# Kernel optimization log

Hardware: AMD Instinct MI355X
Metric: run time of the kernel (lower is better)

Reference implementation:

```python
import jax, jax.numpy as jnp
import numpy as np

N = 262144          # total atoms
B = 2048            # graphs (batch.max()+1)
HID = 256           # hidden
CND = 128           # cond_proj_dim
K = 16              # n_clusters
PH = 8              # pool_heads
DH = HID // PH      # head_dim


def setup_inputs() -> dict:
    key = jax.random.key(0)
    ks = jax.random.split(key, 20)
    s = 0.02
    inp = {
        "h_atom": jax.random.normal(ks[0], (N, HID), jnp.float32),
        "c_atom": jax.random.normal(ks[1], (N, CND), jnp.float32),
        "batch": jnp.sort(jax.random.randint(ks[2], (N,), 0, B)).astype(jnp.int64),
        # gate: Linear(HID+CND, HID) -> GELU -> Linear(HID, 1) -> Sigmoid
        "W1": jax.random.normal(ks[3], (HID + CND, HID), jnp.float32) * s,
        "b1": jnp.zeros((HID,), jnp.float32),
        "W2": jax.random.normal(ks[4], (HID, 1), jnp.float32) * s,
        "b2": jnp.zeros((1,), jnp.float32),
        # assign: Linear(HID, HID) -> GELU -> Linear(HID, K)
        "A1": jax.random.normal(ks[5], (HID, HID), jnp.float32) * s,
        "ab1": jnp.zeros((HID,), jnp.float32),
        "A2": jax.random.normal(ks[6], (HID, K), jnp.float32) * s,
        "ab2": jnp.zeros((K,), jnp.float32),
        # cluster_proj: Linear(HID, HID)
        "Wc": jax.random.normal(ks[7], (HID, HID), jnp.float32) * s,
        "bc": jnp.zeros((HID,), jnp.float32),
        # readout
        "q": jax.random.normal(ks[8], (PH, DH), jnp.float32),   # readout_q param
        "Wk": jax.random.normal(ks[9], (HID, HID), jnp.float32) * s,
        "Wv": jax.random.normal(ks[10], (HID, HID), jnp.float32) * s,
        # LayerNorm
        "gamma": jnp.ones((HID,), jnp.float32),
        "beta": jnp.zeros((HID,), jnp.float32),
    }
    return inp


def reference(h_atom, c_atom, batch, W1, b1, W2, b2, A1, ab1, A2, ab2,
              Wc, bc, q, Wk, Wv, gamma, beta):
    gelu = lambda x: jax.nn.gelu(x, approximate=False)  # torch default GELU (erf)
    # Stage 1: condition-aware gating
    g = gelu(jnp.concatenate([h_atom, c_atom], axis=-1) @ W1 + b1)
    alpha = jax.nn.sigmoid(g @ W2 + b2)                 # [N, 1]
    h_gated = alpha * h_atom                            # [N, HID]
    # Stage 2: soft cluster assignment
    S = jax.nn.softmax(gelu(h_gated @ A1 + ab1) @ A2 + ab2, axis=-1)  # [N, K]
    # Ragged per-graph segment matmul: cluster[b,k,:] = sum_{n in graph b} S[n,k] * h_gated[n,:]
    cluster = jnp.stack(
        [jax.ops.segment_sum(h_gated * S[:, k:k + 1], batch, num_segments=B)
         for k in range(K)], axis=1)                    # [B, K, HID]
    cluster = cluster @ Wc + bc                         # cluster_proj
    # Stage 3: multi-head attention readout over K clusters
    Kp = (cluster @ Wk).reshape(B, K, PH, DH)
    Vp = (cluster @ Wv).reshape(B, K, PH, DH)
    scale = DH ** -0.5
    logits = jnp.einsum('pd,bkpd->bpk', q, Kp) * scale  # [B, PH, K]
    w = jax.nn.softmax(logits, axis=-1)                 # dropout p=0 -> identity
    out = jnp.einsum('bpk,bkpd->bpd', w, Vp).reshape(B, HID)
    # LayerNorm (eps = 1e-5, torch default)
    mu = out.mean(axis=-1, keepdims=True)
    var = ((out - mu) ** 2).mean(axis=-1, keepdims=True)
    return (out - mu) * jax.lax.rsqrt(var + 1e-5) * gamma + beta
```

## Files before the change

### kernel.cpp

```cpp
#include <hip/hip_runtime.h>
#include <hip/hip_bf16.h>
#include <math.h>
#include <stdint.h>

#define NATOMS 262144
#define BGRAPH 2048
#define CHUNK 10240

typedef __bf16 bf16_t;
typedef __bf16 bf16x8 __attribute__((ext_vector_type(8)));
typedef __bf16 bf16x4 __attribute__((ext_vector_type(4)));
typedef float f32x4 __attribute__((ext_vector_type(4)));

__device__ __forceinline__ float bf2f(bf16_t x){ return (float)x; }

__device__ __forceinline__ float gelu_f(float x){
    float s  = x * 0.70710678118654752f;
    float a  = fabsf(s);
    float t  = __builtin_amdgcn_rcpf(fmaf(0.3275911f, a, 1.0f));
    float p  = t * fmaf(t, fmaf(t, fmaf(t, fmaf(t, 1.061405429f, -1.453152027f),
                                        1.421413741f), -0.284496736f), 0.254829592f);
    float e  = __expf(-a * a);
    float er = copysignf(fmaf(-p, e, 1.0f), s);
    return 0.5f * x * (1.0f + er);
}

__device__ __forceinline__ void gl_lds16(const void* g, void* l){
    __attribute__((address_space(3))) uint32_t* lp =
        reinterpret_cast<__attribute__((address_space(3))) uint32_t*>(
            reinterpret_cast<uintptr_t>(l));
    __builtin_amdgcn_global_load_lds(static_cast<const uint32_t*>(g), lp, 16, 0, 0);
}

#define PREP_W1 10
#define PREP_A1 394
#define PREP_WC 650
#define PREP_WK 906
#define PREP_WV 1162
#define PREP_A2 1418
#define PREP_C  1434
#define PREP_END 3482

__device__ __forceinline__ void chunk_tr(const void* src, bf16_t* dst, int Kd, int idx, int bf){
    if (idx >= Kd * 256) return;
    int k = idx >> 8, n = idx & 255;
    bf16_t v = bf ? ((const bf16_t*)src)[idx] : (bf16_t)(((const float*)src)[idx]);
    dst[((size_t)(k >> 5) * 256 + n) * 40 + (k & 31)] = v;
}

__global__ void prep_kernel(
    const int* __restrict__ batch, const void* __restrict__ gamma,
    const void* b1, const void* W2, const void* ab1, const void* bc,
    const void* q, const void* beta, const void* ab2, const void* b2,
    const void* W1, const void* A1, const void* Wc, const void* Wk, const void* Wv,
    const void* A2, const void* cnd,
    bf16_t* __restrict__ W1c, bf16_t* __restrict__ A1c, bf16_t* __restrict__ Wcc,
    bf16_t* __restrict__ Wkc, bf16_t* __restrict__ Wvc, bf16_t* __restrict__ A2t,
    float* __restrict__ P, int* __restrict__ flags, int* __restrict__ starts,
    bf16_t* __restrict__ cbOut)
{
    const int tid = threadIdx.x, blk = blockIdx.x;
    const int bf = (((const unsigned*)gamma)[0] == 0x3F803F80u) ? 1 : 0;
    if (blk == 0 && tid == 0) flags[0] = bf;

    if (blk < 9) {
        int b = blk * 256 + tid;
        if (b > BGRAPH) return;
        int is64 = (batch[NATOMS - 1] == 0) ? 1 : 0;
        int lo = 0, hi = NATOMS;
        while (lo < hi) {
            int mid = (lo + hi) >> 1;
            int v = is64 ? batch[2 * mid] : batch[mid];
            if (v < b) lo = mid + 1; else hi = mid;
        }
        starts[b] = lo;
        return;
    }
    if (blk == 9) {
#define CV(p,i) (bf ? bf2f(((const bf16_t*)(p))[i]) : ((const float*)(p))[i])
        P[tid]        = CV(b1, tid);
        P[256 + tid]  = CV(W2, tid);
        P[512 + tid]  = CV(ab1, tid);
        P[768 + tid]  = CV(bc, tid);
        P[1024 + tid] = CV(q, tid);
        P[1280 + tid] = CV(gamma, tid);
        P[1536 + tid] = CV(beta, tid);
        if (tid < 16) P[1792 + tid] = CV(ab2, tid);
        if (tid == 16) P[1808] = CV(b2, 0);
#undef CV
        return;
    }
    if (blk < PREP_A1) { chunk_tr(W1, W1c, 384, (blk - PREP_W1) * 256 + tid, bf); return; }
    if (blk < PREP_WC) { chunk_tr(A1, A1c, 256, (blk - PREP_A1) * 256 + tid, bf); return; }
    if (blk < PREP_WK) { chunk_tr(Wc, Wcc, 256, (blk - PREP_WC) * 256 + tid, bf); return; }
    if (blk < PREP_WV) { chunk_tr(Wk, Wkc, 256, (blk - PREP_WK) * 256 + tid, bf); return; }
    if (blk < PREP_A2) { chunk_tr(Wv, Wvc, 256, (blk - PREP_WV) * 256 + tid, bf); return; }
    if (blk < PREP_C)  {
        int i = (blk - PREP_A2) * 256 + tid;
        if (i >= 256 * 16) return;
        int k = i >> 4, n = i & 15;
        bf16_t v = bf ? ((const bf16_t*)A2)[i] : (bf16_t)(((const float*)A2)[i]);
        A2t[n * 256 + k] = v;
        return;
    }
    if (bf) return;
    size_t i = (size_t)(blk - PREP_C) * 256 + tid;
    const size_t total = (size_t)NATOMS * 128 / 8;
#pragma unroll
    for (int it = 0; it < 8; ++it, i += 524288) {
        if (i >= total) break;
        const float4* s = (const float4*)cnd + i * 2;
        float4 a = s[0], b = s[1];
        bf16x8 v = { (bf16_t)a.x,(bf16_t)a.y,(bf16_t)a.z,(bf16_t)a.w,
                     (bf16_t)b.x,(bf16_t)b.y,(bf16_t)b.z,(bf16_t)b.w };
        *(bf16x8*)(cbOut + i * 8) = v;
    }
}

__global__ __launch_bounds__(512, 2) void atom_kernel(
    const void* __restrict__ h, const void* __restrict__ cnd, const bf16_t* __restrict__ cb,
    const bf16_t* __restrict__ W1c, const bf16_t* __restrict__ A1c,
    const bf16_t* __restrict__ A2t, const float* __restrict__ P,
    const int* __restrict__ flags,
    bf16_t* __restrict__ hg_out, float* __restrict__ S_out)
{
    __shared__ bf16_t ldsX[128 * 264];
    __shared__ bf16_t ldsW[2][2 * CHUNK];
    __shared__ float  ldsV[256];
    __shared__ float  ldsB1[256];
    __shared__ float  ldsAB1[256];
    __shared__ float  ldsAlpha[128];

    const int tid  = threadIdx.x;
    const int wave = tid >> 6;
    const int lane = tid & 63;
    const int quad = lane >> 4;
    const int l15  = lane & 15;
    const int wr   = wave >> 2;
    const int wc   = wave & 3;
    const int a0   = blockIdx.x * 128;
    const int dbf  = flags[0];

    const bf16_t* cbp = dbf ? (const bf16_t*)cnd : cb;

    bf16x8 cf[4][4];
#pragma unroll
    for (int kc = 0; kc < 4; ++kc)
#pragma unroll
        for (int mt = 0; mt < 4; ++mt)
            cf[kc][mt] = *(const bf16x8*)(cbp + (size_t)(a0 + wr * 64 + mt * 16 + l15) * 128 + kc * 32 + quad * 8);

    if (tid < 256) { ldsV[tid] = P[256 + tid]; ldsB1[tid] = P[tid]; ldsAB1[tid] = P[512 + tid]; }
    if (tid < 128) ldsAlpha[tid] = 0.f;
    const float b2v = P[1808];

    if (dbf) {
        const uint4* hs = (const uint4*)((const bf16_t*)h + (size_t)a0 * 256);
#pragma unroll
        for (int i = 0; i < 8; ++i) {
            int lin = i * 512 + tid; int row = lin >> 5; int off = lin & 31;
            *(uint4*)(&ldsX[row * 264 + off * 8]) = hs[row * 32 + off];
        }
    } else {
        const float4* hs = (const float4*)((const float*)h + (size_t)a0 * 256);
#pragma unroll
        for (int i = 0; i < 16; ++i) {
            int lin = i * 512 + tid; int row = lin >> 6; int off = lin & 63;
            float4 v = hs[row * 64 + off];
            bf16x4 w = { (bf16_t)v.x, (bf16_t)v.y, (bf16_t)v.z, (bf16_t)v.w };
            *(bf16x4*)(&ldsX[row * 264 + off * 4]) = w;
        }
    }

    auto stage = [&](int bsel, const bf16_t* src){
#pragma unroll
        for (int i = 0; i < 5; ++i) {
            int u = i * 512 + wave * 64;
            gl_lds16(src + (size_t)(u + lane) * 8, &ldsW[bsel][0] + (size_t)u * 8);
        }
    };

    stage(0, W1c);
    __syncthreads();

    f32x4 acc[4][4];
#pragma unroll
    for (int a = 0; a < 4; ++a)
#pragma unroll
        for (int b = 0; b < 4; ++b) acc[a][b] = (f32x4){0.f,0.f,0.f,0.f};

#pragma unroll
    for (int ks = 0; ks < 6; ++ks) {
        const int cur = ks & 1;
        const bf16_t* nxt = (ks < 5) ? (W1c + (size_t)(ks + 1) * 2 * CHUNK) : A1c;
        stage(cur ^ 1, nxt);
        bf16x8 af[2][4], bv[2][4];
#pragma unroll
        for (int kh = 0; kh < 2; ++kh)
#pragma unroll
            for (int j = 0; j < 4; ++j)
                bv[kh][j] = *(const bf16x8*)(&ldsW[cur][kh * CHUNK + (wc * 64 + j * 16 + l15) * 40 + quad * 8]);
        if (ks < 4) {
#pragma unroll
            for (int kh = 0; kh < 2; ++kh)
#pragma unroll
                for (int mt = 0; mt < 4; ++mt)
                    af[kh][mt] = *(const bf16x8*)(&ldsX[(wr * 64 + mt * 16 + l15) * 264 + ks * 64 + kh * 32 + quad * 8]);
        } else {
#pragma unroll
            for (int kh = 0; kh < 2; ++kh)
#pragma unroll
                for (int mt = 0; mt < 4; ++mt)
                    af[kh][mt] = cf[(ks - 4) * 2 + kh][mt];
        }
        __builtin_amdgcn_s_setprio(1);
#pragma unroll
        for (int kh = 0; kh < 2; ++kh)
#pragma unroll
            for (int mt = 0; mt < 4; ++mt)
#pragma unroll
                for (int j = 0; j < 4; ++j)
                    acc[mt][j] = __builtin_amdgcn_mfma_f32_16x16x32_bf16(af[kh][mt], bv[kh][j], acc[mt][j], 0, 0, 0);
        __builtin_amdgcn_s_setprio(0);
        __syncthreads();
    }

    for (int mt = 0; mt < 4; ++mt) {
        float p[4] = {0.f, 0.f, 0.f, 0.f};
        for (int j = 0; j < 4; ++j) {
            int col = wc * 64 + j * 16 + l15;
            float w = ldsV[col];
            float bb = ldsB1[col];
            for (int r = 0; r < 4; ++r) {
                float g = gelu_f(acc[mt][j][r] + bb);
                p[r] += g * w;
            }
        }
        for (int off = 1; off < 16; off <<= 1)
            for (int r = 0; r < 4; ++r) p[r] += __shfl_xor(p[r], off, 64);
        if (l15 == 0)
            for (int r = 0; r < 4; ++r)
                atomicAdd(&ldsAlpha[wr * 64 + mt * 16 + quad * 4 + r], p[r]);
    }
    __syncthreads();

    {
        int r = tid >> 2, p4 = tid & 3;
        float al = __builtin_amdgcn_rcpf(1.f + __expf(-(ldsAlpha[r] + b2v)));
        bf16_t* xrow = &ldsX[r * 264 + p4 * 64];
        bf16_t* grow = hg_out + (size_t)(a0 + r) * 256 + p4 * 64;
        for (int i = 0; i < 8; ++i) {
            bf16x8 v = *(bf16x8*)(xrow + i * 8);
            for (int e = 0; e < 8; ++e) v[e] = (bf16_t)(bf2f(v[e]) * al);
            *(bf16x8*)(xrow + i * 8) = v;
            *(bf16x8*)(grow + i * 8) = v;
        }
    }
    __syncthreads();

#pragma unroll
    for (int a = 0; a < 4; ++a)
#pragma unroll
        for (int b = 0; b < 4; ++b) acc[a][b] = (f32x4){0.f,0.f,0.f,0.f};
#pragma unroll
    for (int ks = 0; ks < 4; ++ks) {
        const int cur = ks & 1;
        if (ks < 3) stage(cur ^ 1, A1c + (size_t)(ks + 1) * 2 * CHUNK);
        bf16x8 af[2][4], bv[2][4];
#pragma unroll
        for (int kh = 0; kh < 2; ++kh) {
#pragma unroll
            for (int j = 0; j < 4; ++j)
                bv[kh][j] = *(const bf16x8*)(&ldsW[cur][kh * CHUNK + (wc * 64 + j * 16 + l15) * 40 + quad * 8]);
#pragma unroll
            for (int mt = 0; mt < 4; ++mt)
                af[kh][mt] = *(const bf16x8*)(&ldsX[(wr * 64 + mt * 16 + l15) * 264 + ks * 64 + kh * 32 + quad * 8]);
        }
        __builtin_amdgcn_s_setprio(1);
#pragma unroll
        for (int kh = 0; kh < 2; ++kh)
#pragma unroll
            for (int mt = 0; mt < 4; ++mt)
#pragma unroll
                for (int j = 0; j < 4; ++j)
                    acc[mt][j] = __builtin_amdgcn_mfma_f32_16x16x32_bf16(af[kh][mt], bv[kh][j], acc[mt][j], 0, 0, 0);
        __builtin_amdgcn_s_setprio(0);
        __syncthreads();
    }

    for (int mt = 0; mt < 4; ++mt)
        for (int j = 0; j < 4; ++j) {
            int col = wc * 64 + j * 16 + l15;
            float bb = ldsAB1[col];
            for (int r = 0; r < 4; ++r) {
                int row = wr * 64 + mt * 16 + quad * 4 + r;
                ldsX[row * 264 + col] = (bf16_t)gelu_f(acc[mt][j][r] + bb);
            }
        }
    if (tid < 128) {
        int n = tid >> 3, k0 = (tid & 7) * 32;
#pragma unroll
        for (int p = 0; p < 4; ++p)
            *(uint4*)(&ldsW[0][n * 264 + k0 + p * 8]) = *(const uint4*)(A2t + n * 256 + k0 + p * 8);
    }
    __syncthreads();

    f32x4 acc3 = (f32x4){0.f,0.f,0.f,0.f};
#pragma unroll
    for (int ks = 0; ks < 8; ++ks) {
        int kb = ks * 32 + quad * 8;
        bf16x8 a = *(const bf16x8*)(&ldsX[(wave * 16 + l15) * 264 + kb]);
        bf16x8 b = *(const bf16x8*)(&ldsW[0][l15 * 264 + kb]);
        acc3 = __builtin_amdgcn_mfma_f32_16x16x32_bf16(a, b, acc3, 0, 0, 0);
    }
    float ab2v = P[1792 + l15];
    float lv[4], mx[4], ex[4], sm[4];
    for (int r = 0; r < 4; ++r) { lv[r] = acc3[r] + ab2v; mx[r] = lv[r]; }
    for (int off = 1; off < 16; off <<= 1)
        for (int r = 0; r < 4; ++r) { float o = __shfl_xor(mx[r], off, 64); mx[r] = fmaxf(mx[r], o); }
    for (int r = 0; r < 4; ++r) { ex[r] = __expf(lv[r] - mx[r]); sm[r] = ex[r]; }
    for (int off = 1; off < 16; off <<= 1)
        for (int r = 0; r < 4; ++r) sm[r] += __shfl_xor(sm[r], off, 64);
    for (int r = 0; r < 4; ++r) {
        int row = wave * 16 + quad * 4 + r;
        S_out[(size_t)(a0 + row) * 16 + l15] = ex[r] / sm[r];
    }
}

__global__ __launch_bounds__(256) void segment_kernel(
    const bf16_t* __restrict__ hg, const float* __restrict__ S,
    const int* __restrict__ starts, bf16_t* __restrict__ craw)
{
    __shared__ float ldsS[16 * 16];
    int b = blockIdx.x, tid = threadIdx.x;
    int s = starts[b], e = starts[b + 1];
    float acc[16];
#pragma unroll
    for (int k = 0; k < 16; ++k) acc[k] = 0.f;
    for (int n0 = s; n0 < e; n0 += 16) {
        int cnt = min(16, e - n0);
        if (tid < cnt * 16) ldsS[tid] = S[(size_t)(n0 + (tid >> 4)) * 16 + (tid & 15)];
        __syncthreads();
        for (int a = 0; a < cnt; ++a) {
            float v = bf2f(hg[(size_t)(n0 + a) * 256 + tid]);
            const f32x4* sr = (const f32x4*)(&ldsS[a * 16]);
            f32x4 s0 = sr[0], s1 = sr[1], s2 = sr[2], s3 = sr[3];
            acc[0]  += s0[0] * v; acc[1]  += s0[1] * v; acc[2]  += s0[2] * v; acc[3]  += s0[3] * v;
            acc[4]  += s1[0] * v; acc[5]  += s1[1] * v; acc[6]  += s1[2] * v; acc[7]  += s1[3] * v;
            acc[8]  += s2[0] * v; acc[9]  += s2[1] * v; acc[10] += s2[2] * v; acc[11] += s2[3] * v;
            acc[12] += s3[0] * v; acc[13] += s3[1] * v; acc[14] += s3[2] * v; acc[15] += s3[3] * v;
        }
        __syncthreads();
    }
#pragma unroll
    for (int k = 0; k < 16; ++k)
        craw[((size_t)b * 16 + k) * 256 + tid] = (bf16_t)acc[k];
}

__global__ __launch_bounds__(256, 2) void cluster_kernel(
    const bf16_t* __restrict__ A, const bf16_t* __restrict__ Wcc,
    const bf16_t* __restrict__ Wkc, const bf16_t* __restrict__ Wvc,
    const float* __restrict__ P,
    bf16_t* __restrict__ CK, bf16_t* __restrict__ CV)
{
    __shared__ bf16_t ldsA[64 * 264];
    __shared__ bf16_t ldsW[2][CHUNK];
    const int tid = threadIdx.x;
    const int wave = tid >> 6, lane = tid & 63, quad = lane >> 4, l15 = lane & 15;
    const size_t r0 = (size_t)blockIdx.x * 64;
    const float* bias = P + 768;

    auto stage = [&](int bsel, const bf16_t* src){
#pragma unroll
        for (int i = 0; i < 5; ++i) {
            int u = i * 256 + wave * 64;
            gl_lds16(src + (size_t)(u + lane) * 8, &ldsW[bsel][0] + (size_t)u * 8);
        }
    };

    const uint4* as = (const uint4*)(A + r0 * 256);
#pragma unroll
    for (int i = 0; i < 8; ++i) {
        int lin = i * 256 + tid; int row = lin >> 5; int off = lin & 31;
        *(uint4*)(&ldsA[row * 264 + off * 8]) = as[row * 32 + off];
    }
    stage(0, Wcc);
    __syncthreads();

    f32x4 acc[4][4];

#pragma unroll
    for (int a = 0; a < 4; ++a)
#pragma unroll
        for (int b = 0; b < 4; ++b) acc[a][b] = (f32x4){0.f,0.f,0.f,0.f};
#pragma unroll
    for (int ks = 0; ks < 8; ++ks) {
        const int cur = ks & 1;
        const bf16_t* nxt = (ks < 7) ? (Wcc + (size_t)(ks + 1) * CHUNK) : Wkc;
        stage(cur ^ 1, nxt);
        bf16x8 af[4], bv[4];
        int kb = ks * 32 + quad * 8;
#pragma unroll
        for (int j = 0; j < 4; ++j)
            bv[j] = *(const bf16x8*)(&ldsW[cur][(wave * 64 + j * 16 + l15) * 40 + quad * 8]);
#pragma unroll
        for (int mt = 0; mt < 4; ++mt) af[mt] = *(const bf16x8*)(&ldsA[(mt * 16 + l15) * 264 + kb]);
        __builtin_amdgcn_s_setprio(1);
#pragma unroll
        for (int mt = 0; mt < 4; ++mt)
#pragma unroll
            for (int j = 0; j < 4; ++j)
                acc[mt][j] = __builtin_amdgcn_mfma_f32_16x16x32_bf16(af[mt], bv[j], acc[mt][j], 0, 0, 0);
        __builtin_amdgcn_s_setprio(0);
        __syncthreads();
    }
    for (int mt = 0; mt < 4; ++mt)
        for (int j = 0; j < 4; ++j) {
            int col = wave * 64 + j * 16 + l15;
            float bvl = bias[col];
            for (int r = 0; r < 4; ++r)
                ldsA[(mt * 16 + quad * 4 + r) * 264 + col] = (bf16_t)(acc[mt][j][r] + bvl);
        }
    __syncthreads();

#pragma unroll
    for (int a = 0; a < 4; ++a)
#pragma unroll
        for (int b = 0; b < 4; ++b) acc[a][b] = (f32x4){0.f,0.f,0.f,0.f};
#pragma unroll
    for (int ks = 0; ks < 8; ++ks) {
        const int cur = ks & 1;
        const bf16_t* nxt = (ks < 7) ? (Wkc + (size_t)(ks + 1) * CHUNK) : Wvc;
        stage(cur ^ 1, nxt);
        bf16x8 af[4], bv[4];
        int kb = ks * 32 + quad * 8;
#pragma unroll
        for (int j = 0; j < 4; ++j)
            bv[j] = *(const bf16x8*)(&ldsW[cur][(wave * 64 + j * 16 + l15) * 40 + quad * 8]);
#pragma unroll
        for (int mt = 0; mt < 4; ++mt) af[mt] = *(const bf16x8*)(&ldsA[(mt * 16 + l15) * 264 + kb]);
        __builtin_amdgcn_s_setprio(1);
#pragma unroll
        for (int mt = 0; mt < 4; ++mt)
#pragma unroll
            for (int j = 0; j < 4; ++j)
                acc[mt][j] = __builtin_amdgcn_mfma_f32_16x16x32_bf16(af[mt], bv[j], acc[mt][j], 0, 0, 0);
        __builtin_amdgcn_s_setprio(0);
        __syncthreads();
    }
    for (int mt = 0; mt < 4; ++mt)
        for (int j = 0; j < 4; ++j) {
            int col = wave * 64 + j * 16 + l15;
            for (int r = 0; r < 4; ++r)
                CK[(r0 + mt * 16 + quad * 4 + r) * 256 + col] = (bf16_t)acc[mt][j][r];
        }

#pragma unroll
    for (int a = 0; a < 4; ++a)
#pragma unroll
        for (int b = 0; b < 4; ++b) acc[a][b] = (f32x4){0.f,0.f,0.f,0.f};
#pragma unroll
    for (int ks = 0; ks < 8; ++ks) {
        const int cur = ks & 1;
        if (ks < 7) stage(cur ^ 1, Wvc + (size_t)(ks + 1) * CHUNK);
        bf16x8 af[4], bv[4];
        int kb = ks * 32 + quad * 8;
#pragma unroll
        for (int j = 0; j < 4; ++j)
            bv[j] = *(const bf16x8*)(&ldsW[cur][(wave * 64 + j * 16 + l15) * 40 + quad * 8]);
#pragma unroll
        for (int mt = 0; mt < 4; ++mt) af[mt] = *(const bf16x8*)(&ldsA[(mt * 16 + l15) * 264 + kb]);
        __builtin_amdgcn_s_setprio(1);
#pragma unroll
        for (int mt = 0; mt < 4; ++mt)
#pragma unroll
            for (int j = 0; j < 4; ++j)
                acc[mt][j] = __builtin_amdgcn_mfma_f32_16x16x32_bf16(af[mt], bv[j], acc[mt][j], 0, 0, 0);
        __builtin_amdgcn_s_setprio(0);
        __syncthreads();
    }
    for (int mt = 0; mt < 4; ++mt)
        for (int j = 0; j < 4; ++j) {
            int col = wave * 64 + j * 16 + l15;
            for (int r = 0; r < 4; ++r)
                CV[(r0 + mt * 16 + quad * 4 + r) * 256 + col] = (bf16_t)acc[mt][j][r];
        }
}

__global__ __launch_bounds__(256) void attn_ln_kernel(
    const bf16_t* __restrict__ Kp, const bf16_t* __restrict__ Vp,
    const float* __restrict__ P, const int* __restrict__ flags,
    void* __restrict__ out)
{
    __shared__ float lw[8][16];
    __shared__ float w1s[4], w2s[4];
    int b = blockIdx.x, tid = threadIdx.x;
    const int dbf = flags[0];
    const float* q     = P + 1024;
    const float* gamma = P + 1280;
    const float* beta  = P + 1536;
    if (tid < 128) {
        int p = tid >> 4, k = tid & 15;
        const bf16x8* kr = (const bf16x8*)(Kp + ((size_t)b * 16 + k) * 256 + p * 32);
        const float* qr = q + p * 32;
        float dot = 0.f;
#pragma unroll
        for (int i = 0; i < 4; ++i) {
            bf16x8 v = kr[i];
#pragma unroll
            for (int e = 0; e < 8; ++e) dot += qr[i * 8 + e] * bf2f(v[e]);
        }
        lw[p][k] = dot * 0.17677669529663687f;
    }
    __syncthreads();
    if (tid < 8) {
        float m = -1e30f;
        for (int k = 0; k < 16; ++k) m = fmaxf(m, lw[tid][k]);
        float s = 0.f;
        for (int k = 0; k < 16; ++k) { float ev = __expf(lw[tid][k] - m); lw[tid][k] = ev; s += ev; }
        float inv = 1.f / s;
        for (int k = 0; k < 16; ++k) lw[tid][k] *= inv;
    }
    __syncthreads();
    int p = tid >> 5, d = tid & 31;
    float o = 0.f;
    for (int k = 0; k < 16; ++k)
        o += lw[p][k] * bf2f(Vp[((size_t)b * 16 + k) * 256 + p * 32 + d]);
    float s1 = o, s2 = o * o;
    for (int off = 1; off < 64; off <<= 1) { s1 += __shfl_xor(s1, off, 64); s2 += __shfl_xor(s2, off, 64); }
    int wv = tid >> 6;
    if ((tid & 63) == 0) { w1s[wv] = s1; w2s[wv] = s2; }
    __syncthreads();
    float ts1 = w1s[0] + w1s[1] + w1s[2] + w1s[3];
    float ts2 = w2s[0] + w2s[1] + w2s[2] + w2s[3];
    float mu = ts1 * (1.f / 256.f);
    float var = ts2 * (1.f / 256.f) - mu * mu;
    float y = (o - mu) * rsqrtf(var + 1e-5f) * gamma[tid] + beta[tid];
    if (dbf) ((bf16_t*)out)[(size_t)b * 256 + tid] = (bf16_t)y;
    else     ((float*)out)[(size_t)b * 256 + tid]  = y;
}

extern "C" void kernel_launch(void* const* d_in, const int* in_sizes, int n_in,
                              void* d_out, int out_size, void* d_ws, size_t ws_size,
                              hipStream_t stream) {
    const void* h     = d_in[0];
    const void* cnd   = d_in[1];
    const int*  batch = (const int*)d_in[2];
    const void* W1    = d_in[3];
    const void* b1    = d_in[4];
    const void* W2    = d_in[5];
    const void* b2    = d_in[6];
    const void* A1    = d_in[7];
    const void* ab1   = d_in[8];
    const void* A2    = d_in[9];
    const void* ab2   = d_in[10];
    const void* Wc    = d_in[11];
    const void* bc    = d_in[12];
    const void* q     = d_in[13];
    const void* Wk    = d_in[14];
    const void* Wv    = d_in[15];
    const void* gamma = d_in[16];
    const void* beta  = d_in[17];

    char* ws = (char*)d_ws;
    size_t off = 0;
    bf16_t* W1c  = (bf16_t*)(ws + off); off += 12 * CHUNK * 2;
    bf16_t* A1c  = (bf16_t*)(ws + off); off += 8 * CHUNK * 2;
    bf16_t* Wcc  = (bf16_t*)(ws + off); off += 8 * CHUNK * 2;
    bf16_t* Wkc  = (bf16_t*)(ws + off); off += 8 * CHUNK * 2;
    bf16_t* Wvc  = (bf16_t*)(ws + off); off += 8 * CHUNK * 2;
    bf16_t* A2t  = (bf16_t*)(ws + off); off += 8192;
    float*  P    = (float*)(ws + off);  off += 8192;
    int*    flags = (int*)(ws + off);   off += 256;
    int*    starts = (int*)(ws + off);  off += 8448;
    float*  S    = (float*)(ws + off);  off += (size_t)NATOMS * 16 * 4;
    bf16_t* hg   = (bf16_t*)(ws + off); off += (size_t)NATOMS * 256 * 2;
    bf16_t* craw = (bf16_t*)(ws + off); off += (size_t)BGRAPH * 16 * 256 * 2;
    bf16_t* padA = (bf16_t*)(ws + off); off += (size_t)BGRAPH * 16 * 256 * 2;
    bf16_t* KpB  = (bf16_t*)(ws + off); off += (size_t)BGRAPH * 16 * 256 * 2;
    bf16_t* VpB  = (bf16_t*)(ws + off); off += (size_t)BGRAPH * 16 * 256 * 2;
    bf16_t* cb   = craw;
    (void)padA; (void)ws_size; (void)n_in; (void)in_sizes; (void)out_size;

    prep_kernel<<<PREP_END, 256, 0, stream>>>(
        batch, gamma, b1, W2, ab1, bc, q, beta, ab2, b2,
        W1, A1, Wc, Wk, Wv, A2, cnd,
        W1c, A1c, Wcc, Wkc, Wvc, A2t, P, flags, starts, cb);

    atom_kernel<<<NATOMS / 128, 512, 0, stream>>>(h, cnd, cb, W1c, A1c, A2t, P, flags, hg, S);
    segment_kernel<<<BGRAPH, 256, 0, stream>>>(hg, S, starts, craw);
    cluster_kernel<<<BGRAPH * 16 / 64, 256, 0, stream>>>(craw, Wcc, Wkc, Wvc, P, KpB, VpB);
    attn_ln_kernel<<<BGRAPH, 256, 0, stream>>>(KpB, VpB, P, flags, d_out);
}
```

Measured before the change: 807.6 us.

## Restructure atom kernel per-wave weight stripes, fold alpha into A1 GEMM, batch segment loads

After: 806.5 us. About the same (-0.1%).

```diff
diff --git a/kernel.cpp b/kernel.cpp
--- a/kernel.cpp
+++ b/kernel.cpp
@@ -38,8 +38,7 @@
 #define PREP_WK 906
 #define PREP_WV 1162
 #define PREP_A2 1418
-#define PREP_C  1434
-#define PREP_END 3482
+#define PREP_END 1434
 
 __device__ __forceinline__ void chunk_tr(const void* src, bf16_t* dst, int Kd, int idx, int bf){
     if (idx >= Kd * 256) return;
@@ -53,11 +52,10 @@
     const void* b1, const void* W2, const void* ab1, const void* bc,
     const void* q, const void* beta, const void* ab2, const void* b2,
     const void* W1, const void* A1, const void* Wc, const void* Wk, const void* Wv,
-    const void* A2, const void* cnd,
+    const void* A2,
     bf16_t* __restrict__ W1c, bf16_t* __restrict__ A1c, bf16_t* __restrict__ Wcc,
     bf16_t* __restrict__ Wkc, bf16_t* __restrict__ Wvc, bf16_t* __restrict__ A2t,
-    float* __restrict__ P, int* __restrict__ flags, int* __restrict__ starts,
-    bf16_t* __restrict__ cbOut)
+    float* __restrict__ P, int* __restrict__ flags, int* __restrict__ starts)
 {
     const int tid = threadIdx.x, blk = blockIdx.x;
     const int bf = (((const unsigned*)gamma)[0] == 0x3F803F80u) ? 1 : 0;
@@ -95,92 +93,95 @@
     if (blk < PREP_WK) { chunk_tr(Wc, Wcc, 256, (blk - PREP_WC) * 256 + tid, bf); return; }
     if (blk < PREP_WV) { chunk_tr(Wk, Wkc, 256, (blk - PREP_WK) * 256 + tid, bf); return; }
     if (blk < PREP_A2) { chunk_tr(Wv, Wvc, 256, (blk - PREP_WV) * 256 + tid, bf); return; }
-    if (blk < PREP_C)  {
+    {
         int i = (blk - PREP_A2) * 256 + tid;
         if (i >= 256 * 16) return;
         int k = i >> 4, n = i & 15;
         bf16_t v = bf ? ((const bf16_t*)A2)[i] : (bf16_t)(((const float*)A2)[i]);
         A2t[n * 256 + k] = v;
-        return;
-    }
-    if (bf) return;
-    size_t i = (size_t)(blk - PREP_C) * 256 + tid;
-    const size_t total = (size_t)NATOMS * 128 / 8;
-#pragma unroll
-    for (int it = 0; it < 8; ++it, i += 524288) {
-        if (i >= total) break;
-        const float4* s = (const float4*)cnd + i * 2;
-        float4 a = s[0], b = s[1];
-        bf16x8 v = { (bf16_t)a.x,(bf16_t)a.y,(bf16_t)a.z,(bf16_t)a.w,
-                     (bf16_t)b.x,(bf16_t)b.y,(bf16_t)b.z,(bf16_t)b.w };
-        *(bf16x8*)(cbOut + i * 8) = v;
-    }
-}
-
-__global__ __launch_bounds__(512, 2) void atom_kernel(
-    const void* __restrict__ h, const void* __restrict__ cnd, const bf16_t* __restrict__ cb,
+    }
+}
+
+__global__ __launch_bounds__(256, 2) void atom_kernel(
+    const void* __restrict__ h, const void* __restrict__ cnd,
     const bf16_t* __restrict__ W1c, const bf16_t* __restrict__ A1c,
     const bf16_t* __restrict__ A2t, const float* __restrict__ P,
     const int* __restrict__ flags,
     bf16_t* __restrict__ hg_out, float* __restrict__ S_out)
 {
-    __shared__ bf16_t ldsX[128 * 264];
-    __shared__ bf16_t ldsW[2][2 * CHUNK];
-    __shared__ float  ldsV[256];
-    __shared__ float  ldsB1[256];
-    __shared__ float  ldsAB1[256];
-    __shared__ float  ldsAlpha[128];
+    __shared__ bf16_t ldsX[64 * 264];
+    __shared__ bf16_t ldsW[4 * 2 * 2560];
+    __shared__ float  ldsAlpha[64];
 
     const int tid  = threadIdx.x;
     const int wave = tid >> 6;
     const int lane = tid & 63;
     const int quad = lane >> 4;
     const int l15  = lane & 15;
-    const int wr   = wave >> 2;
-    const int wc   = wave & 3;
-    const int a0   = blockIdx.x * 128;
+    const int a0   = blockIdx.x * 64;
     const int dbf  = flags[0];
-
-    const bf16_t* cbp = dbf ? (const bf16_t*)cnd : cb;
+    bf16_t* stripe = &ldsW[wave * 5120];
+    bf16_t* ldsT   = &ldsW[0];
+
+    float b1r[4], w2r[4], ab1r[4];
+#pragma unroll
+    for (int j = 0; j < 4; ++j) {
+        int col = wave * 64 + j * 16 + l15;
+        b1r[j]  = P[col];
+        w2r[j]  = P[256 + col];
+        ab1r[j] = P[512 + col];
+    }
+    const float b2v = P[1808];
+    if (tid < 64) ldsAlpha[tid] = 0.f;
 
     bf16x8 cf[4][4];
-#pragma unroll
-    for (int kc = 0; kc < 4; ++kc)
-#pragma unroll
-        for (int mt = 0; mt < 4; ++mt)
-            cf[kc][mt] = *(const bf16x8*)(cbp + (size_t)(a0 + wr * 64 + mt * 16 + l15) * 128 + kc * 32 + quad * 8);
-
-    if (tid < 256) { ldsV[tid] = P[256 + tid]; ldsB1[tid] = P[tid]; ldsAB1[tid] = P[512 + tid]; }
-    if (tid < 128) ldsAlpha[tid] = 0.f;
-    const float b2v = P[1808];
+    if (dbf) {
+#pragma unroll
+        for (int kc = 0; kc < 4; ++kc)
+#pragma unroll
+            for (int mt = 0; mt < 4; ++mt)
+                cf[kc][mt] = *(const bf16x8*)((const bf16_t*)cnd +
+                    (size_t)(a0 + mt * 16 + l15) * 128 + kc * 32 + quad * 8);
+    } else {
+#pragma unroll
+        for (int kc = 0; kc < 4; ++kc)
+#pragma unroll
+            for (int mt = 0; mt < 4; ++mt) {
+                const float* cp = (const float*)cnd +
+                    (size_t)(a0 + mt * 16 + l15) * 128 + kc * 32 + quad * 8;
+                float4 u0 = *(const float4*)cp;
+                float4 u1 = *(const float4*)(cp + 4);
+                cf[kc][mt] = (bf16x8){ (bf16_t)u0.x,(bf16_t)u0.y,(bf16_t)u0.z,(bf16_t)u0.w,
+                                       (bf16_t)u1.x,(bf16_t)u1.y,(bf16_t)u1.z,(bf16_t)u1.w };
+            }
+    }
 
     if (dbf) {
         const uint4* hs = (const uint4*)((const bf16_t*)h + (size_t)a0 * 256);
 #pragma unroll
         for (int i = 0; i < 8; ++i) {
-            int lin = i * 512 + tid; int row = lin >> 5; int off = lin & 31;
+            int lin = i * 256 + tid; int row = lin >> 5; int off = lin & 31;
             *(uint4*)(&ldsX[row * 264 + off * 8]) = hs[row * 32 + off];
         }
     } else {
         const float4* hs = (const float4*)((const float*)h + (size_t)a0 * 256);
 #pragma unroll
         for (int i = 0; i < 16; ++i) {
-            int lin = i * 512 + tid; int row = lin >> 6; int off = lin & 63;
+            int lin = i * 256 + tid; int row = lin >> 6; int off = lin & 63;
             float4 v = hs[row * 64 + off];
             bf16x4 w = { (bf16_t)v.x, (bf16_t)v.y, (bf16_t)v.z, (bf16_t)v.w };
             *(bf16x4*)(&ldsX[row * 264 + off * 4]) = w;
         }
     }
 
-    auto stage = [&](int bsel, const bf16_t* src){
-#pragma unroll
-        for (int i = 0; i < 5; ++i) {
-            int u = i * 512 + wave * 64;
-            gl_lds16(src + (size_t)(u + lane) * 8, &ldsW[bsel][0] + (size_t)u * 8);
-        }
+    auto stageW = [&](int bsel, const bf16_t* chunk){
+#pragma unroll
+        for (int i = 0; i < 5; ++i)
+            gl_lds16(chunk + (size_t)wave * 2560 + i * 512 + lane * 8,
+                     stripe + bsel * 2560 + i * 512);
     };
 
-    stage(0, W1c);
+    stageW(0, W1c);
     __syncthreads();
 
     f32x4 acc[4][4];
@@ -190,128 +191,113 @@
         for (int b = 0; b < 4; ++b) acc[a][b] = (f32x4){0.f,0.f,0.f,0.f};
 
 #pragma unroll
-    for (int ks = 0; ks < 6; ++ks) {
+    for (int ks = 0; ks < 12; ++ks) {
         const int cur = ks & 1;
-        const bf16_t* nxt = (ks < 5) ? (W1c + (size_t)(ks + 1) * 2 * CHUNK) : A1c;
-        stage(cur ^ 1, nxt);
-        bf16x8 af[2][4], bv[2][4];
-#pragma unroll
-        for (int kh = 0; kh < 2; ++kh)
+        const bf16_t* nxt = (ks < 11) ? (W1c + (size_t)(ks + 1) * CHUNK) : A1c;
+        stageW(cur ^ 1, nxt);
+        asm volatile("s_waitcnt vmcnt(5)" ::: "memory");
+        bf16x8 af[4], bv[4];
+#pragma unroll
+        for (int j = 0; j < 4; ++j)
+            bv[j] = *(const bf16x8*)(stripe + cur * 2560 + (j * 16 + l15) * 40 + quad * 8);
+        if (ks < 8) {
+            int kb = ks * 32 + quad * 8;
+#pragma unroll
+            for (int mt = 0; mt < 4; ++mt) af[mt] = *(const bf16x8*)(&ldsX[(mt * 16 + l15) * 264 + kb]);
+        } else {
+#pragma unroll
+            for (int mt = 0; mt < 4; ++mt) af[mt] = cf[ks - 8][mt];
+        }
+        __builtin_amdgcn_s_setprio(1);
+#pragma unroll
+        for (int mt = 0; mt < 4; ++mt)
 #pragma unroll
             for (int j = 0; j < 4; ++j)
-                bv[kh][j] = *(const bf16x8*)(&ldsW[cur][kh * CHUNK + (wc * 64 + j * 16 + l15) * 40 + quad * 8]);
-        if (ks < 4) {
-#pragma unroll
-            for (int kh = 0; kh < 2; ++kh)
-#pragma unroll
-                for (int mt = 0; mt < 4; ++mt)
-                    af[kh][mt] = *(const bf16x8*)(&ldsX[(wr * 64 + mt * 16 + l15) * 264 + ks * 64 + kh * 32 + quad * 8]);
-        } else {
-#pragma unroll
-            for (int kh = 0; kh < 2; ++kh)
-#pragma unroll
-                for (int mt = 0; mt < 4; ++mt)
-                    af[kh][mt] = cf[(ks - 4) * 2 + kh][mt];
-        }
-        __builtin_amdgcn_s_setprio(1);
-#pragma unroll
-        for (int kh = 0; kh < 2; ++kh)
-#pragma unroll
-            for (int mt = 0; mt < 4; ++mt)
-#pragma unroll
-                for (int j = 0; j < 4; ++j)
-                    acc[mt][j] = __builtin_amdgcn_mfma_f32_16x16x32_bf16(af[kh][mt], bv[kh][j], acc[mt][j], 0, 0, 0);
+                acc[mt][j] = __builtin_amdgcn_mfma_f32_16x16x32_bf16(af[mt], bv[j], acc[mt][j], 0, 0, 0);
         __builtin_amdgcn_s_setprio(0);
-        __syncthreads();
     }
 
     for (int mt = 0; mt < 4; ++mt) {
         float p[4] = {0.f, 0.f, 0.f, 0.f};
         for (int j = 0; j < 4; ++j) {
-            int col = wc * 64 + j * 16 + l15;
-            float w = ldsV[col];
-            float bb = ldsB1[col];
             for (int r = 0; r < 4; ++r) {
-                float g = gelu_f(acc[mt][j][r] + bb);
-                p[r] += g * w;
+                float g = gelu_f(acc[mt][j][r] + b1r[j]);
+                p[r] += g * w2r[j];
             }
         }
         for (int off = 1; off < 16; off <<= 1)
             for (int r = 0; r < 4; ++r) p[r] += __shfl_xor(p[r], off, 64);
         if (l15 == 0)
             for (int r = 0; r < 4; ++r)
-                atomicAdd(&ldsAlpha[wr * 64 + mt * 16 + quad * 4 + r], p[r]);
-    }
+                atomicAdd(&ldsAlpha[mt * 16 + quad * 4 + r], p[r]);
+    }
+
+    f32x4 acc2[4][4];
+#pragma unroll
+    for (int a = 0; a < 4; ++a)
+#pragma unroll
+        for (int b = 0; b < 4; ++b) acc2[a][b] = (f32x4){0.f,0.f,0.f,0.f};
+#pragma unroll
+    for (int ks = 0; ks < 8; ++ks) {
+        const int cur = ks & 1;
+        if (ks < 7) {
+            stageW(cur ^ 1, A1c + (size_t)(ks + 1) * CHUNK);
+            asm volatile("s_waitcnt vmcnt(5)" ::: "memory");
+        } else {
+            asm volatile("s_waitcnt vmcnt(0)" ::: "memory");
+        }
+        bf16x8 af[4], bv[4];
+        int kb = ks * 32 + quad * 8;
+#pragma unroll
+        for (int j = 0; j < 4; ++j)
+            bv[j] = *(const bf16x8*)(stripe + cur * 2560 + (j * 16 + l15) * 40 + quad * 8);
+#pragma unroll
+        for (int mt = 0; mt < 4; ++mt) af[mt] = *(const bf16x8*)(&ldsX[(mt * 16 + l15) * 264 + kb]);
+        __builtin_amdgcn_s_setprio(1);
+#pragma unroll
+        for (int mt = 0; mt < 4; ++mt)
+#pragma unroll
+            for (int j = 0; j < 4; ++j)
+                acc2[mt][j] = __builtin_amdgcn_mfma_f32_16x16x32_bf16(af[mt], bv[j], acc2[mt][j], 0, 0, 0);
+        __builtin_amdgcn_s_setprio(0);
+    }
+
     __syncthreads();
 
     {
         int r = tid >> 2, p4 = tid & 3;
         float al = __builtin_amdgcn_rcpf(1.f + __expf(-(ldsAlpha[r] + b2v)));
-        bf16_t* xrow = &ldsX[r * 264 + p4 * 64];
+        const bf16_t* xrow = &ldsX[r * 264 + p4 * 64];
         bf16_t* grow = hg_out + (size_t)(a0 + r) * 256 + p4 * 64;
         for (int i = 0; i < 8; ++i) {
-            bf16x8 v = *(bf16x8*)(xrow + i * 8);
+            bf16x8 v = *(const bf16x8*)(xrow + i * 8);
             for (int e = 0; e < 8; ++e) v[e] = (bf16_t)(bf2f(v[e]) * al);
-            *(bf16x8*)(xrow + i * 8) = v;
             *(bf16x8*)(grow + i * 8) = v;
         }
-    }
-    __syncthreads();
-
-#pragma unroll
-    for (int a = 0; a < 4; ++a)
-#pragma unroll
-        for (int b = 0; b < 4; ++b) acc[a][b] = (f32x4){0.f,0.f,0.f,0.f};
-#pragma unroll
-    for (int ks = 0; ks < 4; ++ks) {
-        const int cur = ks & 1;
-        if (ks < 3) stage(cur ^ 1, A1c + (size_t)(ks + 1) * 2 * CHUNK);
-        bf16x8 af[2][4], bv[2][4];
-#pragma unroll
-        for (int kh = 0; kh < 2; ++kh) {
-#pragma unroll
-            for (int j = 0; j < 4; ++j)
-                bv[kh][j] = *(const bf16x8*)(&ldsW[cur][kh * CHUNK + (wc * 64 + j * 16 + l15) * 40 + quad * 8]);
-#pragma unroll
-            for (int mt = 0; mt < 4; ++mt)
-                af[kh][mt] = *(const bf16x8*)(&ldsX[(wr * 64 + mt * 16 + l15) * 264 + ks * 64 + kh * 32 + quad * 8]);
-        }
-        __builtin_amdgcn_s_setprio(1);
-#pragma unroll
-        for (int kh = 0; kh < 2; ++kh)
-#pragma unroll
-            for (int mt = 0; mt < 4; ++mt)
-#pragma unroll
-                for (int j = 0; j < 4; ++j)
-                    acc[mt][j] = __builtin_amdgcn_mfma_f32_16x16x32_bf16(af[kh][mt], bv[kh][j], acc[mt][j], 0, 0, 0);
-        __builtin_amdgcn_s_setprio(0);
-        __syncthreads();
     }
 
     for (int mt = 0; mt < 4; ++mt)
         for (int j = 0; j < 4; ++j) {
-            int col = wc * 64 + j * 16 + l15;
-            float bb = ldsAB1[col];
+            int col = wave * 64 + j * 16 + l15;
             for (int r = 0; r < 4; ++r) {
-                int row = wr * 64 + mt * 16 + quad * 4 + r;
-                ldsX[row * 264 + col] = (bf16_t)gelu_f(acc[mt][j][r] + bb);
+                int row = mt * 16 + quad * 4 + r;
+                float al = __builtin_amdgcn_rcpf(1.f + __expf(-(ldsAlpha[row] + b2v)));
+                ldsT[row * 264 + col] = (bf16_t)gelu_f(al * acc2[mt][j][r] + ab1r[j]);
             }
         }
-    if (tid < 128) {
-        int n = tid >> 3, k0 = (tid & 7) * 32;
-#pragma unroll
-        for (int p = 0; p < 4; ++p)
-            *(uint4*)(&ldsW[0][n * 264 + k0 + p * 8]) = *(const uint4*)(A2t + n * 256 + k0 + p * 8);
-    }
+
+    bf16x8 a2r[8];
+#pragma unroll
+    for (int ks = 0; ks < 8; ++ks)
+        a2r[ks] = *(const bf16x8*)(A2t + l15 * 256 + ks * 32 + quad * 8);
+
     __syncthreads();
 
     f32x4 acc3 = (f32x4){0.f,0.f,0.f,0.f};
 #pragma unroll
     for (int ks = 0; ks < 8; ++ks) {
-        int kb = ks * 32 + quad * 8;
-        bf16x8 a = *(const bf16x8*)(&ldsX[(wave * 16 + l15) * 264 + kb]);
-        bf16x8 b = *(const bf16x8*)(&ldsW[0][l15 * 264 + kb]);
-        acc3 = __builtin_amdgcn_mfma_f32_16x16x32_bf16(a, b, acc3, 0, 0, 0);
+        bf16x8 a = *(const bf16x8*)(&ldsT[(wave * 16 + l15) * 264 + ks * 32 + quad * 8]);
+        acc3 = __builtin_amdgcn_mfma_f32_16x16x32_bf16(a, a2r[ks], acc3, 0, 0, 0);
     }
     float ab2v = P[1792 + l15];
     float lv[4], mx[4], ex[4], sm[4];
@@ -331,24 +317,38 @@
     const bf16_t* __restrict__ hg, const float* __restrict__ S,
     const int* __restrict__ starts, bf16_t* __restrict__ craw)
 {
-    __shared__ float ldsS[16 * 16];
+    __shared__ float ldsS[64 * 16];
     int b = blockIdx.x, tid = threadIdx.x;
     int s = starts[b], e = starts[b + 1];
     float acc[16];
 #pragma unroll
     for (int k = 0; k < 16; ++k) acc[k] = 0.f;
-    for (int n0 = s; n0 < e; n0 += 16) {
-        int cnt = min(16, e - n0);
-        if (tid < cnt * 16) ldsS[tid] = S[(size_t)(n0 + (tid >> 4)) * 16 + (tid & 15)];
+    for (int n0 = s; n0 < e; n0 += 64) {
+        int na = e - n0;
+#pragma unroll
+        for (int i = 0; i < 4; ++i) {
+            int idx = i * 256 + tid;
+            int a = idx >> 4, k = idx & 15;
+            ldsS[idx] = (a < na) ? S[(size_t)(n0 + a) * 16 + k] : 0.f;
+        }
         __syncthreads();
-        for (int a = 0; a < cnt; ++a) {
-            float v = bf2f(hg[(size_t)(n0 + a) * 256 + tid]);
-            const f32x4* sr = (const f32x4*)(&ldsS[a * 16]);
-            f32x4 s0 = sr[0], s1 = sr[1], s2 = sr[2], s3 = sr[3];
-            acc[0]  += s0[0] * v; acc[1]  += s0[1] * v; acc[2]  += s0[2] * v; acc[3]  += s0[3] * v;
-            acc[4]  += s1[0] * v; acc[5]  += s1[1] * v; acc[6]  += s1[2] * v; acc[7]  += s1[3] * v;
-            acc[8]  += s2[0] * v; acc[9]  += s2[1] * v; acc[10] += s2[2] * v; acc[11] += s2[3] * v;
-            acc[12] += s3[0] * v; acc[13] += s3[1] * v; acc[14] += s3[2] * v; acc[15] += s3[3] * v;
+        int gmax = (min(na, 64) + 15) >> 4;
+        for (int g = 0; g < gmax; ++g) {
+            float v[16];
+#pragma unroll
+            for (int a = 0; a < 16; ++a) {
+                int n = n0 + g * 16 + a;
+                v[a] = (n < e) ? bf2f(hg[(size_t)n * 256 + tid]) : 0.f;
+            }
+#pragma unroll
+            for (int a = 0; a < 16; ++a) {
+                const f32x4* sr = (const f32x4*)(&ldsS[(g * 16 + a) * 16]);
+                f32x4 s0 = sr[0], s1 = sr[1], s2 = sr[2], s3 = sr[3];
+                acc[0]  += s0[0] * v[a]; acc[1]  += s0[1] * v[a]; acc[2]  += s0[2] * v[a]; acc[3]  += s0[3] * v[a];
+                acc[4]  += s1[0] * v[a]; acc[5]  += s1[1] * v[a]; acc[6]  += s1[2] * v[a]; acc[7]  += s1[3] * v[a];
+                acc[8]  += s2[0] * v[a]; acc[9]  += s2[1] * v[a]; acc[10] += s2[2] * v[a]; acc[11] += s2[3] * v[a];
+                acc[12] += s3[0] * v[a]; acc[13] += s3[1] * v[a]; acc[14] += s3[2] * v[a]; acc[15] += s3[3] * v[a];
+            }
         }
         __syncthreads();
     }
@@ -576,18 +576,16 @@
     float*  S    = (float*)(ws + off);  off += (size_t)NATOMS * 16 * 4;
     bf16_t* hg   = (bf16_t*)(ws + off); off += (size_t)NATOMS * 256 * 2;
     bf16_t* craw = (bf16_t*)(ws + off); off += (size_t)BGRAPH * 16 * 256 * 2;
-    bf16_t* padA = (bf16_t*)(ws + off); off += (size_t)BGRAPH * 16 * 256 * 2;
     bf16_t* KpB  = (bf16_t*)(ws + off); off += (size_t)BGRAPH * 16 * 256 * 2;
     bf16_t* VpB  = (bf16_t*)(ws + off); off += (size_t)BGRAPH * 16 * 256 * 2;
-    bf16_t* cb   = craw;
-    (void)padA; (void)ws_size; (void)n_in; (void)in_sizes; (void)out_size;
+    (void)ws_size; (void)n_in; (void)in_sizes; (void)out_size;
 
     prep_kernel<<<PREP_END, 256, 0, stream>>>(
         batch, gamma, b1, W2, ab1, bc, q, beta, ab2, b2,
-        W1, A1, Wc, Wk, Wv, A2, cnd,
-        W1c, A1c, Wcc, Wkc, Wvc, A2t, P, flags, starts, cb);
-
-    atom_kernel<<<NATOMS / 128, 512, 0, stream>>>(h, cnd, cb, W1c, A1c, A2t, P, flags, hg, S);
+        W1, A1, Wc, Wk, Wv, A2,
+        W1c, A1c, Wcc, Wkc, Wvc, A2t, P, flags, starts);
+
+    atom_kernel<<<NATOMS / 64, 256, 0, stream>>>(h, cnd, W1c, A1c, A2t, P, flags, hg, S);
     segment_kernel<<<BGRAPH, 256, 0, stream>>>(hg, S, starts, craw);
     cluster_kernel<<<BGRAPH * 16 / 64, 256, 0, stream>>>(craw, Wcc, Wkc, Wvc, P, KpB, VpB);
     attn_ln_kernel<<<BGRAPH, 256, 0, stream>>>(KpB, VpB, P, flags, d_out);
```
